# Optimization experiments

Hardware: AMD Instinct MI355X
Metric: run time of the kernel (lower is better)

The kernel has to match this reference:

```python
import jax, jax.numpy as jnp
import numpy as np

DIM, KEY_DIM, HEADS, RATIO, RES = 384, 32, 8, 4, 7
N = RES * RES
D = RATIO * KEY_DIM          # 128 per-head value dim
DH = D * HEADS               # 1024
NHKD = KEY_DIM * HEADS       # 256
SCALE = KEY_DIM ** -0.5


def _make_bias_idxs(res):
    points = [(i, j) for i in range(res) for j in range(res)]
    offsets = {}
    idxs = []
    for p1 in points:
        for p2 in points:
            off = (abs(p1[0] - p2[0]), abs(p1[1] - p2[1]))
            if off not in offsets:
                offsets[off] = len(offsets)
            idxs.append(offsets[off])
    n = len(points)
    return np.asarray(idxs, dtype=np.int32).reshape(n, n), len(offsets)


def setup_inputs() -> dict:
    key = jax.random.key(0)
    ks = jax.random.split(key, 10)
    B = 2048
    idxs_np, n_off = _make_bias_idxs(RES)
    s = 0.02
    return {
        "x": jax.random.normal(ks[0], (B, N, DIM), jnp.float32),
        "q_w": jax.random.normal(ks[1], (NHKD, DIM), jnp.float32) * s,
        "q_b": jnp.zeros((NHKD,), jnp.float32),
        "k_w": jax.random.normal(ks[2], (NHKD, DIM), jnp.float32) * s,
        "k_b": jnp.zeros((NHKD,), jnp.float32),
        "v_w": jax.random.normal(ks[3], (DH, DIM), jnp.float32) * s,
        "v_b": jnp.zeros((DH,), jnp.float32),
        "proj_w": jax.random.normal(ks[4], (DIM, DH), jnp.float32) * s,
        "proj_b": jnp.zeros((DIM,), jnp.float32),
        "attention_biases": jax.random.normal(ks[5], (HEADS, n_off), jnp.float32) * s,
        "bias_idxs": jnp.asarray(idxs_np),  # [N, N] int32
    }


def reference(x, q_w, q_b, k_w, k_b, v_w, v_b, proj_w, proj_b,
              attention_biases, bias_idxs):
    B, n, _ = x.shape
    q = (x @ q_w.T + q_b).reshape(B, n, HEADS, KEY_DIM)
    k = (x @ k_w.T + k_b).reshape(B, n, HEADS, KEY_DIM)
    v = (x @ v_w.T + v_b).reshape(B, n, HEADS, D)
    # learned relative-position bias gathered per (query, key) pair: [H, N, N]
    ab = attention_biases[:, bias_idxs]
    attn = jnp.einsum("bnhd,bmhd->bhnm", q, k) * SCALE + ab
    attn = jax.nn.softmax(attn, axis=-1)
    out = jnp.einsum("bhnm,bmhd->bnhd", attn, v).reshape(B, n, DH)
    return out @ proj_w.T + proj_b
```

## Files before the change

kernel.cpp:

```cpp
#include <hip/hip_runtime.h>
#include <hip/hip_bf16.h>

#define NTOK   49
#define DIM    384
#define KEY_DIM 32
#define HEADS  8
#define D_HEAD 128
#define SCALE  0.17677669529663687f

typedef short short8 __attribute__((ext_vector_type(8)));
typedef short short4_t __attribute__((ext_vector_type(4)));
typedef float f32x4 __attribute__((ext_vector_type(4)));

__device__ __forceinline__ unsigned short f2bf(float x) {
    union { __hip_bfloat16 b; unsigned short u; } v;
    v.b = __float2bfloat16(x);
    return v.u;
}

__device__ __forceinline__ f32x4 MFMA(short8 a, short8 b, f32x4 c) {
    return __builtin_amdgcn_mfma_f32_16x16x32_bf16(a, b, c, 0, 0, 0);
}

__device__ __forceinline__ void bar_lgkm() {
    asm volatile("s_waitcnt lgkmcnt(0)" ::: "memory");
    __builtin_amdgcn_sched_barrier(0);
    __builtin_amdgcn_s_barrier();
    __builtin_amdgcn_sched_barrier(0);
}

__global__ void prologue(const float* __restrict__ qw, const float* __restrict__ qb,
                         const float* __restrict__ kw,
                         const float* __restrict__ vw, const float* __restrict__ pw,
                         const float* __restrict__ biases, const int* __restrict__ idxs,
                         int n_off,
                         unsigned short* __restrict__ qk_p,
                         unsigned short* __restrict__ vw_p,
                         unsigned short* __restrict__ pw_p,
                         float* __restrict__ qb_s,
                         float* __restrict__ ab_t) {
    int t = blockIdx.x * 256 + threadIdx.x;
    if (t < 24576) {
        int lane = t & 63, kt = (t >> 6) % 12, ntile = t / 768;
        int c = ntile * 16 + (lane & 15), kk = kt * 32 + (lane >> 4) * 8;
        const float* src = (c < 256) ? (qw + c * 384 + kk) : (kw + (c - 256) * 384 + kk);
        float sc = (c < 256) ? SCALE : 1.0f;
        short8 o;
#pragma unroll
        for (int j = 0; j < 8; ++j) o[j] = (short)f2bf(src[j] * sc);
        *(short8*)(qk_p + (size_t)t * 8) = o;
    } else if (t < 73728) {
        int u = t - 24576;
        int lane = u & 63, kt = (u >> 6) % 12, ntile = u / 768;
        int c = ntile * 16 + (lane & 15), kk = kt * 32 + (lane >> 4) * 8;
        const float* src = vw + c * 384 + kk;
        short8 o;
#pragma unroll
        for (int j = 0; j < 8; ++j) o[j] = (short)f2bf(src[j]);
        *(short8*)(vw_p + (size_t)u * 8) = o;
    } else if (t < 122880) {
        int u = t - 73728;
        int lane = u & 63, kt = (u >> 6) % 32, ntile = u / 2048;
        int c = ntile * 16 + (lane & 15), kk = kt * 32 + (lane >> 4) * 8;
        const float* src = pw + c * 1024 + kk;
        short8 o;
#pragma unroll
        for (int j = 0; j < 8; ++j) o[j] = (short)f2bf(src[j]);
        *(short8*)(pw_p + (size_t)u * 8) = o;
    } else if (t < 123136) {
        int u = t - 122880;
        qb_s[u] = qb[u] * SCALE;
    } else if (t < 123136 + 32768) {
        int u = t - 123136;
        int h = u >> 12, n = (u >> 6) & 63, m = u & 63;
        float v = 0.f;
        if (m < 49 && n < 49) v = biases[h * n_off + idxs[n * 49 + m]];
        ab_t[u] = v;
    }
}

__global__ __launch_bounds__(512, 4) void attn_qkv(
        const float* __restrict__ x,
        const unsigned short* __restrict__ qkw,
        const unsigned short* __restrict__ vw,
        const float* __restrict__ qb_s, const float* __restrict__ kb,
        const float* __restrict__ vb,
        const float* __restrict__ ab_t,
        unsigned short* __restrict__ O_p) {

    __shared__ __align__(16) unsigned short smem[37072];
    unsigned short* xs  = smem;
    unsigned short* ps  = smem + 19208;
    unsigned short* vsT = smem + 22736;
    unsigned short* qs  = smem + 31952;
    unsigned short* ks2 = smem + 34512;

    const int tid  = threadIdx.x;
    const int lane = tid & 63;
    const int wid  = tid >> 6;
    const int l15  = lane & 15;
    const int lg   = lane >> 4;
    const int b    = blockIdx.x;

    const float* xb = x + (size_t)b * (NTOK * DIM);
#pragma unroll 2
    for (int i = tid; i < 4704; i += 512) {
        f32x4 v = __builtin_nontemporal_load(((const f32x4*)xb) + i);
        int f = i * 4;
        int row = f / DIM;
        int col = f - row * DIM;
        short4_t pk;
        pk[0] = (short)f2bf(v[0]); pk[1] = (short)f2bf(v[1]);
        pk[2] = (short)f2bf(v[2]); pk[3] = (short)f2bf(v[3]);
        *(short4_t*)&xs[row * 392 + col] = pk;
    }
    __syncthreads();

    const f32x4 zf = (f32x4)0.f;

    for (int h = 0; h < HEADS; ++h) {
        {
            const int mh  = wid >> 2;
            const int nt0 = 3 * (wid & 3);
            const int rA0 = min(mh * 32 + l15, 48);
            const int rA1 = min(mh * 32 + 16 + l15, 48);
            f32x4 acc[3][2];
#pragma unroll
            for (int i = 0; i < 3; ++i) { acc[i][0] = zf; acc[i][1] = zf; }

            const short8* bptr[3];
#pragma unroll
            for (int i = 0; i < 3; ++i) {
                int nt = nt0 + i;
                const unsigned short* base; int ntile;
                if (nt < 2)      { base = qkw; ntile = 2 * h + nt; }
                else if (nt < 4) { base = qkw; ntile = 16 + 2 * h + (nt - 2); }
                else             { base = vw;  ntile = 8 * h + (nt - 4); }
                bptr[i] = (const short8*)(base + (size_t)ntile * 12 * 64 * 8);
            }
            __builtin_amdgcn_s_setprio(1);
#pragma unroll
            for (int kt = 0; kt < 12; ++kt) {
                short8 a0 = *(const short8*)&xs[rA0 * 392 + kt * 32 + lg * 8];
                short8 a1 = *(const short8*)&xs[rA1 * 392 + kt * 32 + lg * 8];
#pragma unroll
                for (int i = 0; i < 3; ++i) {
                    short8 bf = bptr[i][kt * 64 + lane];
                    acc[i][0] = MFMA(a0, bf, acc[i][0]);
                    acc[i][1] = MFMA(a1, bf, acc[i][1]);
                }
            }
            __builtin_amdgcn_s_setprio(0);
#pragma unroll
            for (int i = 0; i < 3; ++i) {
                int nt = nt0 + i;
                int c  = nt * 16 + l15;
                if (nt < 4) {
                    int cc = (nt < 2) ? c : c - 32;
                    float bias = (nt < 2) ? qb_s[h * 32 + cc] : kb[h * 32 + cc];
                    unsigned short* dst = (nt < 2) ? qs : ks2;
#pragma unroll
                    for (int j = 0; j < 2; ++j) {
                        int r0 = mh * 32 + j * 16 + lg * 4;
                        f32x4 v = acc[i][j];
#pragma unroll
                        for (int r = 0; r < 4; ++r)
                            dst[(r0 + r) * 40 + cc] = f2bf(v[r] + bias);
                    }
                } else {
                    int d = c - 64;
                    float bias = vb[h * 128 + d];
#pragma unroll
                    for (int j = 0; j < 2; ++j) {
                        int m0 = mh * 32 + j * 16 + lg * 4;
                        f32x4 v = acc[i][j];
                        short4_t pk;
#pragma unroll
                        for (int r = 0; r < 4; ++r) pk[r] = (short)f2bf(v[r] + bias);
                        *(short4_t*)&vsT[d * 72 + m0] = pk;
                    }
                }
            }
        }
        bar_lgkm();

        if (wid < 4) {
            const int I = wid;
            const int rq = min(I * 16 + l15, 48);
            short8 bq = *(const short8*)&qs[rq * 40 + lg * 8];
            f32x4 s[4];
#pragma unroll
            for (int J = 0; J < 4; ++J) {
                short8 ak = *(const short8*)&ks2[(J * 16 + l15) * 40 + lg * 8];
                s[J] = MFMA(ak, bq, zf);
            }
            const f32x4* abn = (const f32x4*)(ab_t + ((h * 64 + I * 16 + l15) * 64));
            float sv[16];
            float mx = -1e30f;
#pragma unroll
            for (int J = 0; J < 4; ++J) {
                f32x4 a4 = abn[J * 4 + lg];
#pragma unroll
                for (int r = 0; r < 4; ++r) {
                    int m = J * 16 + lg * 4 + r;
                    float val = s[J][r] + a4[r];
                    if (m >= 49) val = -1e30f;
                    sv[J * 4 + r] = val;
                    mx = fmaxf(mx, val);
                }
            }
            mx = fmaxf(mx, __shfl_xor(mx, 16));
            mx = fmaxf(mx, __shfl_xor(mx, 32));
            float sum = 0.f;
#pragma unroll
            for (int t = 0; t < 16; ++t) { float e = __expf(sv[t] - mx); sv[t] = e; sum += e; }
            sum += __shfl_xor(sum, 16);
            sum += __shfl_xor(sum, 32);
            float inv = 1.0f / sum;
            int n = I * 16 + l15;
            if (n < 49) {
#pragma unroll
                for (int J = 0; J < 4; ++J)
#pragma unroll
                    for (int r = 0; r < 4; ++r) {
                        int m = J * 16 + lg * 4 + r;
                        ps[n * 72 + m] = f2bf(sv[J * 4 + r] * inv);
                    }
            }
        }
        bar_lgkm();

        {
            const int np = wid >> 2;
            const int dp = wid & 3;
            const int rp0 = min(np * 32 + l15, 48);
            const int rp1 = min(np * 32 + 16 + l15, 48);
            f32x4 a00 = zf, a01 = zf, a10 = zf, a11 = zf;
            __builtin_amdgcn_s_setprio(1);
#pragma unroll
            for (int kk = 0; kk < 2; ++kk) {
                short8 a0 = *(const short8*)&ps[rp0 * 72 + kk * 32 + lg * 8];
                short8 a1 = *(const short8*)&ps[rp1 * 72 + kk * 32 + lg * 8];
                short8 b0 = *(const short8*)&vsT[(dp * 32 + l15) * 72 + kk * 32 + lg * 8];
                short8 b1 = *(const short8*)&vsT[(dp * 32 + 16 + l15) * 72 + kk * 32 + lg * 8];
                a00 = MFMA(a0, b0, a00); a01 = MFMA(a0, b1, a01);
                a10 = MFMA(a1, b0, a10); a11 = MFMA(a1, b1, a11);
            }
            __builtin_amdgcn_s_setprio(0);
            f32x4 accs[2][2] = {{a00, a01}, {a10, a11}};
            unsigned short* ob = O_p + (((size_t)b * 8 + h) * 32) * 256;
#pragma unroll
            for (int jn = 0; jn < 2; ++jn)
#pragma unroll
                for (int jd = 0; jd < 2; ++jd) {
                    int frag = (np * 2 + jn) * 8 + (dp * 2 + jd);
                    f32x4 v = accs[jn][jd];
                    short4_t pk;
#pragma unroll
                    for (int r = 0; r < 4; ++r) pk[r] = (short)f2bf(v[r]);
                    __builtin_nontemporal_store(pk, (short4_t*)(ob + frag * 256 + lane * 4));
                }
        }
        bar_lgkm();
    }
}

#define OPJ_STRIDE 520
__global__ __launch_bounds__(512, 4) void out_proj(
        const unsigned short* __restrict__ O_p,
        const unsigned short* __restrict__ pw,
        const float* __restrict__ pb,
        float* __restrict__ out) {

    __shared__ unsigned short osB[64 * OPJ_STRIDE];

    const int tid  = threadIdx.x;
    const int lane = tid & 63;
    const int wid  = tid >> 6;
    const int l15  = lane & 15;
    const int lg   = lane >> 4;
    const int b    = blockIdx.x;

    const short8* pwp = (const short8*)pw;
    f32x4 acc[3][4];
#pragma unroll
    for (int i = 0; i < 3; ++i)
#pragma unroll
        for (int I = 0; I < 4; ++I) acc[i][I] = (f32x4)0.f;

#pragma unroll
    for (int p = 0; p < 2; ++p) {
        const short8* obase = (const short8*)(O_p + (size_t)b * 65536 + p * 32768);
        short8 vv[8];
#pragma unroll
        for (int it = 0; it < 8; ++it)
            vv[it] = __builtin_nontemporal_load(obase + tid + it * 512);
        if (p) __syncthreads();
#pragma unroll
        for (int it = 0; it < 8; ++it) {
            int s = tid + it * 512;
            int fl0 = s * 2;
            int hl   = fl0 >> 11;
            int frag = (fl0 >> 6) & 31;
            int ln0  = fl0 & 63;
            int mt = frag >> 3, dt = frag & 7;
            short8 v = vv[it];
#pragma unroll
            for (int q = 0; q < 2; ++q) {
                int ln = ln0 + q;
                int n0 = mt * 16 + ((ln >> 4) << 2);
                int d  = hl * 128 + dt * 16 + (ln & 15);
#pragma unroll
                for (int r = 0; r < 4; ++r)
                    osB[(n0 + r) * OPJ_STRIDE + d] = (unsigned short)v[q * 4 + r];
            }
        }
        __syncthreads();

        for (int ktl = 0; ktl < 16; ++ktl) {
            short8 bfr[4];
#pragma unroll
            for (int I = 0; I < 4; ++I)
                bfr[I] = *(const short8*)&osB[(I * 16 + l15) * OPJ_STRIDE + ktl * 32 + lg * 8];
#pragma unroll
            for (int i = 0; i < 3; ++i) {
                short8 a = pwp[((size_t)(wid * 3 + i) * 32 + p * 16 + ktl) * 64 + lane];
#pragma unroll
                for (int I = 0; I < 4; ++I) acc[i][I] = MFMA(a, bfr[I], acc[i][I]);
            }
        }
    }

    float* obaseo = out + (size_t)b * (NTOK * 384);
#pragma unroll
    for (int i = 0; i < 3; ++i) {
        int c0 = (wid * 3 + i) * 16 + lg * 4;
        f32x4 bias4 = *(const f32x4*)&pb[c0];
#pragma unroll
        for (int I = 0; I < 4; ++I) {
            int n = I * 16 + l15;
            if (n < 49) {
                f32x4 v = acc[i][I] + bias4;
                __builtin_nontemporal_store(v, (f32x4*)&obaseo[n * 384 + c0]);
            }
        }
    }
}

__global__ __launch_bounds__(512) void fused_attn(
        const float* __restrict__ x,
        const unsigned short* __restrict__ qkw,
        const unsigned short* __restrict__ vw,
        const unsigned short* __restrict__ pw,
        const float* __restrict__ qb_s, const float* __restrict__ kb,
        const float* __restrict__ vb, const float* __restrict__ pb,
        const float* __restrict__ ab_t,
        float* __restrict__ out) {

    __shared__ __align__(16) unsigned short smem[40656];
    unsigned short* xs  = smem;
    unsigned short* ps  = smem + 19208;
    unsigned short* vsT = smem + 22736;
    unsigned short* qs  = smem + 31952;
    unsigned short* ks2 = smem + 31952 + 2560;
    unsigned short* osA = smem + 31952;

    const int tid  = threadIdx.x;
    const int lane = tid & 63;
    const int wid  = tid >> 6;
    const int l15  = lane & 15;
    const int lg   = lane >> 4;
    const int b    = blockIdx.x;

    const float* xb = x + (size_t)b * (NTOK * DIM);
#pragma unroll 2
    for (int i = tid; i < 4704; i += 512) {
        f32x4 v = __builtin_nontemporal_load(((const f32x4*)xb) + i);
        int f = i * 4;
        int row = f / DIM;
        int col = f - row * DIM;
        short4_t pk;
        pk[0] = (short)f2bf(v[0]); pk[1] = (short)f2bf(v[1]);
        pk[2] = (short)f2bf(v[2]); pk[3] = (short)f2bf(v[3]);
        *(short4_t*)&xs[row * 392 + col] = pk;
    }
    __syncthreads();

    f32x4 pacc[3][4];
#pragma unroll
    for (int i = 0; i < 3; ++i)
#pragma unroll
        for (int j = 0; j < 4; ++j) pacc[i][j] = (f32x4)0.f;

    const f32x4 zf = (f32x4)0.f;

    for (int h = 0; h < HEADS; ++h) {
        {
            const int mh  = wid >> 2;
            const int nt0 = 3 * (wid & 3);
            const int rA0 = min(mh * 32 + l15, 48);
            const int rA1 = min(mh * 32 + 16 + l15, 48);
            f32x4 acc[3][2];
#pragma unroll
            for (int i = 0; i < 3; ++i) { acc[i][0] = zf; acc[i][1] = zf; }

            const short8* bptr[3];
#pragma unroll
            for (int i = 0; i < 3; ++i) {
                int nt = nt0 + i;
                const unsigned short* base; int ntile;
                if (nt < 2)      { base = qkw; ntile = 2 * h + nt; }
                else if (nt < 4) { base = qkw; ntile = 16 + 2 * h + (nt - 2); }
                else             { base = vw;  ntile = 8 * h + (nt - 4); }
                bptr[i] = (const short8*)(base + (size_t)ntile * 12 * 64 * 8);
            }
#pragma unroll
            for (int kt = 0; kt < 12; ++kt) {
                short8 a0 = *(const short8*)&xs[rA0 * 392 + kt * 32 + lg * 8];
                short8 a1 = *(const short8*)&xs[rA1 * 392 + kt * 32 + lg * 8];
#pragma unroll
                for (int i = 0; i < 3; ++i) {
                    short8 bf = bptr[i][kt * 64 + lane];
                    acc[i][0] = MFMA(a0, bf, acc[i][0]);
                    acc[i][1] = MFMA(a1, bf, acc[i][1]);
                }
            }
#pragma unroll
            for (int i = 0; i < 3; ++i) {
                int nt = nt0 + i;
                int c  = nt * 16 + l15;
                if (nt < 4) {
                    int cc = (nt < 2) ? c : c - 32;
                    float bias = (nt < 2) ? qb_s[h * 32 + cc] : kb[h * 32 + cc];
                    unsigned short* dst = (nt < 2) ? qs : ks2;
#pragma unroll
                    for (int j = 0; j < 2; ++j) {
                        int r0 = mh * 32 + j * 16 + lg * 4;
                        f32x4 v = acc[i][j];
#pragma unroll
                        for (int r = 0; r < 4; ++r)
                            dst[(r0 + r) * 40 + cc] = f2bf(v[r] + bias);
                    }
                } else {
                    int d = c - 64;
                    float bias = vb[h * 128 + d];
#pragma unroll
                    for (int j = 0; j < 2; ++j) {
                        int m0 = mh * 32 + j * 16 + lg * 4;
                        f32x4 v = acc[i][j];
                        short4_t pk;
#pragma unroll
                        for (int r = 0; r < 4; ++r) pk[r] = (short)f2bf(v[r] + bias);
                        *(short4_t*)&vsT[d * 72 + m0] = pk;
                    }
                }
            }
        }
        __syncthreads();

        if (wid < 4) {
            const int I = wid;
            const int rq = min(I * 16 + l15, 48);
            short8 bq = *(const short8*)&qs[rq * 40 + lg * 8];
            f32x4 s[4];
#pragma unroll
            for (int J = 0; J < 4; ++J) {
                short8 ak = *(const short8*)&ks2[(J * 16 + l15) * 40 + lg * 8];
                s[J] = MFMA(ak, bq, zf);
            }
            const f32x4* abn = (const f32x4*)(ab_t + ((h * 64 + I * 16 + l15) * 64));
            float sv[16];
            float mx = -1e30f;
#pragma unroll
            for (int J = 0; J < 4; ++J) {
                f32x4 a4 = abn[J * 4 + lg];
#pragma unroll
                for (int r = 0; r < 4; ++r) {
                    int m = J * 16 + lg * 4 + r;
                    float val = s[J][r] + a4[r];
                    if (m >= 49) val = -1e30f;
                    sv[J * 4 + r] = val;
                    mx = fmaxf(mx, val);
                }
            }
            mx = fmaxf(mx, __shfl_xor(mx, 16));
            mx = fmaxf(mx, __shfl_xor(mx, 32));
            float sum = 0.f;
#pragma unroll
            for (int t = 0; t < 16; ++t) { float e = __expf(sv[t] - mx); sv[t] = e; sum += e; }
            sum += __shfl_xor(sum, 16);
            sum += __shfl_xor(sum, 32);
            float inv = 1.0f / sum;
            int n = I * 16 + l15;
            if (n < 49) {
#pragma unroll
                for (int J = 0; J < 4; ++J)
#pragma unroll
                    for (int r = 0; r < 4; ++r) {
                        int m = J * 16 + lg * 4 + r;
                        ps[n * 72 + m] = f2bf(sv[J * 4 + r] * inv);
                    }
            }
        }
        __syncthreads();

        {
            const int np = wid >> 2;
            const int dp = wid & 3;
            const int rp0 = min(np * 32 + l15, 48);
            const int rp1 = min(np * 32 + 16 + l15, 48);
            f32x4 a00 = zf, a01 = zf, a10 = zf, a11 = zf;
#pragma unroll
            for (int kk = 0; kk < 2; ++kk) {
                short8 a0 = *(const short8*)&ps[rp0 * 72 + kk * 32 + lg * 8];
                short8 a1 = *(const short8*)&ps[rp1 * 72 + kk * 32 + lg * 8];
                short8 b0 = *(const short8*)&vsT[(dp * 32 + l15) * 72 + kk * 32 + lg * 8];
                short8 b1 = *(const short8*)&vsT[(dp * 32 + 16 + l15) * 72 + kk * 32 + lg * 8];
                a00 = MFMA(a0, b0, a00); a01 = MFMA(a0, b1, a01);
                a10 = MFMA(a1, b0, a10); a11 = MFMA(a1, b1, a11);
            }
            f32x4 accs[2][2] = {{a00, a01}, {a10, a11}};
#pragma unroll
            for (int jn = 0; jn < 2; ++jn)
#pragma unroll
                for (int jd = 0; jd < 2; ++jd) {
                    int r0 = np * 32 + jn * 16 + lg * 4;
                    int d0 = dp * 32 + jd * 16 + l15;
                    f32x4 v = accs[jn][jd];
#pragma unroll
                    for (int r = 0; r < 4; ++r) osA[(r0 + r) * 136 + d0] = f2bf(v[r]);
                }
        }
        __syncthreads();

        {
            const int nt0 = 3 * wid;
#pragma unroll
            for (int kt = 0; kt < 4; ++kt) {
                short8 a[4];
#pragma unroll
                for (int mi = 0; mi < 4; ++mi)
                    a[mi] = *(const short8*)&osA[(mi * 16 + l15) * 136 + kt * 32 + lg * 8];
#pragma unroll
                for (int i = 0; i < 3; ++i) {
                    short8 bf = ((const short8*)pw)[((size_t)(nt0 + i) * 32 + (h * 4 + kt)) * 64 + lane];
#pragma unroll
                    for (int mi = 0; mi < 4; ++mi)
                        pacc[i][mi] = MFMA(a[mi], bf, pacc[i][mi]);
                }
            }
        }
        __syncthreads();
    }

    float* ob = out + (size_t)b * (NTOK * 384);
#pragma unroll
    for (int i = 0; i < 3; ++i) {
        int c = (3 * wid + i) * 16 + l15;
        float bias = pb[c];
#pragma unroll
        for (int mi = 0; mi < 4; ++mi) {
            f32x4 v = pacc[i][mi];
#pragma unroll
            for (int r = 0; r < 4; ++r) {
                int n = mi * 16 + lg * 4 + r;
                if (n < 49) __builtin_nontemporal_store(v[r] + bias, &ob[n * 384 + c]);
            }
        }
    }
}

extern "C" void kernel_launch(void* const* d_in, const int* in_sizes, int n_in,
                              void* d_out, int out_size, void* d_ws, size_t ws_size,
                              hipStream_t stream) {
    const float* x      = (const float*)d_in[0];
    const float* qw     = (const float*)d_in[1];
    const float* qb     = (const float*)d_in[2];
    const float* kw     = (const float*)d_in[3];
    const float* kb     = (const float*)d_in[4];
    const float* vw     = (const float*)d_in[5];
    const float* vb     = (const float*)d_in[6];
    const float* pw     = (const float*)d_in[7];
    const float* pb     = (const float*)d_in[8];
    const float* biases = (const float*)d_in[9];
    const int*   idxs   = (const int*)d_in[10];
    int n_off = in_sizes[9] / HEADS;

    char* ws = (char*)d_ws;
    unsigned short* qk_p = (unsigned short*)ws;
    unsigned short* vw_p = (unsigned short*)(ws + 393216);
    unsigned short* pw_p = (unsigned short*)(ws + 1179648);
    float*          qb_s = (float*)(ws + 1966080);
    float*          ab_t = (float*)(ws + 1967104);
    unsigned short* O_p  = (unsigned short*)(ws + 2098176);

    const size_t need = 2098176ull + (size_t)2048 * 8 * 32 * 256 * 2;

    prologue<<<609, 256, 0, stream>>>(qw, qb, kw, vw, pw, biases, idxs, n_off,
                                      qk_p, vw_p, pw_p, qb_s, ab_t);
    if (ws_size >= need) {
        attn_qkv<<<2048, 512, 0, stream>>>(x, qk_p, vw_p, qb_s, kb, vb, ab_t, O_p);
        out_proj<<<2048, 512, 0, stream>>>(O_p, pw_p, pb, (float*)d_out);
    } else {
        fused_attn<<<2048, 512, 0, stream>>>(x, qk_p, vw_p, pw_p, qb_s, kb, vb, pb,
                                             ab_t, (float*)d_out);
    }
}
```

Before: 414.8 us.

## Warp-specialize attention heads to overlap projections with softmax and PV

Splits the eight waves into two roles per head. Waves 0-3 run softmax and then the P·V product. Meanwhile waves 4-7 compute the V projection for the current head, and then the Q/K projections for the next head. The Q/K projection for head 0 is hoisted before the loop. This removes one block barrier per head and hides the projection MFMAs behind the softmax and PV phases. The cost is uneven per-wave work and more accumulator registers per wave.

Measured after the change: 435.3 us. 5.0% more time.

```diff
diff --git a/kernel.cpp b/kernel.cpp
--- a/kernel.cpp
+++ b/kernel.cpp
@@ -118,70 +118,36 @@
 
     const f32x4 zf = (f32x4)0.f;
 
+    {
+        const int nt  = wid >> 1;
+        const int mtb = (wid & 1) * 2;
+        const int ntile = (nt < 2) ? nt : (16 + (nt - 2));
+        const short8* bptr = (const short8*)(qkw + (size_t)ntile * 12 * 64 * 8);
+        const int rA0 = min(mtb * 16 + l15, 48);
+        const int rA1 = min(mtb * 16 + 16 + l15, 48);
+        f32x4 a0c = zf, a1c = zf;
+#pragma unroll
+        for (int kt = 0; kt < 12; ++kt) {
+            short8 a0 = *(const short8*)&xs[rA0 * 392 + kt * 32 + lg * 8];
+            short8 a1 = *(const short8*)&xs[rA1 * 392 + kt * 32 + lg * 8];
+            short8 bf = bptr[kt * 64 + lane];
+            a0c = MFMA(a0, bf, a0c);
+            a1c = MFMA(a1, bf, a1c);
+        }
+        const int cc = (nt & 1) * 16 + l15;
+        float bias = (nt < 2) ? qb_s[cc] : kb[cc];
+        unsigned short* dst = (nt < 2) ? qs : ks2;
+        f32x4 accs[2] = {a0c, a1c};
+#pragma unroll
+        for (int j = 0; j < 2; ++j) {
+            int r0 = (mtb + j) * 16 + lg * 4;
+#pragma unroll
+            for (int r = 0; r < 4; ++r)
+                dst[(r0 + r) * 40 + cc] = f2bf(accs[j][r] + bias);
+        }
+    }
+
     for (int h = 0; h < HEADS; ++h) {
-        {
-            const int mh  = wid >> 2;
-            const int nt0 = 3 * (wid & 3);
-            const int rA0 = min(mh * 32 + l15, 48);
-            const int rA1 = min(mh * 32 + 16 + l15, 48);
-            f32x4 acc[3][2];
-#pragma unroll
-            for (int i = 0; i < 3; ++i) { acc[i][0] = zf; acc[i][1] = zf; }
-
-            const short8* bptr[3];
-#pragma unroll
-            for (int i = 0; i < 3; ++i) {
-                int nt = nt0 + i;
-                const unsigned short* base; int ntile;
-                if (nt < 2)      { base = qkw; ntile = 2 * h + nt; }
-                else if (nt < 4) { base = qkw; ntile = 16 + 2 * h + (nt - 2); }
-                else             { base = vw;  ntile = 8 * h + (nt - 4); }
-                bptr[i] = (const short8*)(base + (size_t)ntile * 12 * 64 * 8);
-            }
-            __builtin_amdgcn_s_setprio(1);
-#pragma unroll
-            for (int kt = 0; kt < 12; ++kt) {
-                short8 a0 = *(const short8*)&xs[rA0 * 392 + kt * 32 + lg * 8];
-                short8 a1 = *(const short8*)&xs[rA1 * 392 + kt * 32 + lg * 8];
-#pragma unroll
-                for (int i = 0; i < 3; ++i) {
-                    short8 bf = bptr[i][kt * 64 + lane];
-                    acc[i][0] = MFMA(a0, bf, acc[i][0]);
-                    acc[i][1] = MFMA(a1, bf, acc[i][1]);
-                }
-            }
-            __builtin_amdgcn_s_setprio(0);
-#pragma unroll
-            for (int i = 0; i < 3; ++i) {
-                int nt = nt0 + i;
-                int c  = nt * 16 + l15;
-                if (nt < 4) {
-                    int cc = (nt < 2) ? c : c - 32;
-                    float bias = (nt < 2) ? qb_s[h * 32 + cc] : kb[h * 32 + cc];
-                    unsigned short* dst = (nt < 2) ? qs : ks2;
-#pragma unroll
-                    for (int j = 0; j < 2; ++j) {
-                        int r0 = mh * 32 + j * 16 + lg * 4;
-                        f32x4 v = acc[i][j];
-#pragma unroll
-                        for (int r = 0; r < 4; ++r)
-                            dst[(r0 + r) * 40 + cc] = f2bf(v[r] + bias);
-                    }
-                } else {
-                    int d = c - 64;
-                    float bias = vb[h * 128 + d];
-#pragma unroll
-                    for (int j = 0; j < 2; ++j) {
-                        int m0 = mh * 32 + j * 16 + lg * 4;
-                        f32x4 v = acc[i][j];
-                        short4_t pk;
-#pragma unroll
-                        for (int r = 0; r < 4; ++r) pk[r] = (short)f2bf(v[r] + bias);
-                        *(short4_t*)&vsT[d * 72 + m0] = pk;
-                    }
-                }
-            }
-        }
         bar_lgkm();
 
         if (wid < 4) {
@@ -227,41 +193,120 @@
                         ps[n * 72 + m] = f2bf(sv[J * 4 + r] * inv);
                     }
             }
+        } else {
+            const int w = wid - 4;
+            const short8* bp0 = (const short8*)(vw + (size_t)(8 * h + 2 * w) * 12 * 64 * 8);
+            const short8* bp1 = (const short8*)(vw + (size_t)(8 * h + 2 * w + 1) * 12 * 64 * 8);
+            f32x4 acc[2][4];
+#pragma unroll
+            for (int i = 0; i < 2; ++i)
+#pragma unroll
+                for (int m = 0; m < 4; ++m) acc[i][m] = zf;
+            const int r0 = l15, r1 = 16 + l15, r2 = 32 + l15, r3 = 48;
+            __builtin_amdgcn_s_setprio(1);
+#pragma unroll
+            for (int kt = 0; kt < 12; ++kt) {
+                short8 a0 = *(const short8*)&xs[r0 * 392 + kt * 32 + lg * 8];
+                short8 a1 = *(const short8*)&xs[r1 * 392 + kt * 32 + lg * 8];
+                short8 a2 = *(const short8*)&xs[r2 * 392 + kt * 32 + lg * 8];
+                short8 a3 = *(const short8*)&xs[r3 * 392 + kt * 32 + lg * 8];
+                short8 b0 = bp0[kt * 64 + lane];
+                short8 b1 = bp1[kt * 64 + lane];
+                acc[0][0] = MFMA(a0, b0, acc[0][0]); acc[0][1] = MFMA(a1, b0, acc[0][1]);
+                acc[0][2] = MFMA(a2, b0, acc[0][2]); acc[0][3] = MFMA(a3, b0, acc[0][3]);
+                acc[1][0] = MFMA(a0, b1, acc[1][0]); acc[1][1] = MFMA(a1, b1, acc[1][1]);
+                acc[1][2] = MFMA(a2, b1, acc[1][2]); acc[1][3] = MFMA(a3, b1, acc[1][3]);
+            }
+            __builtin_amdgcn_s_setprio(0);
+#pragma unroll
+            for (int i = 0; i < 2; ++i) {
+                int d = (2 * w + i) * 16 + l15;
+                float bias = vb[h * 128 + d];
+#pragma unroll
+                for (int mt = 0; mt < 4; ++mt) {
+                    int m0 = mt * 16 + lg * 4;
+                    short4_t pk;
+#pragma unroll
+                    for (int r = 0; r < 4; ++r) pk[r] = (short)f2bf(acc[i][mt][r] + bias);
+                    *(short4_t*)&vsT[d * 72 + m0] = pk;
+                }
+            }
         }
         bar_lgkm();
 
-        {
-            const int np = wid >> 2;
-            const int dp = wid & 3;
+        if (wid < 4) {
+            const int np  = wid >> 1;
+            const int dpb = (wid & 1) * 2;
             const int rp0 = min(np * 32 + l15, 48);
             const int rp1 = min(np * 32 + 16 + l15, 48);
-            f32x4 a00 = zf, a01 = zf, a10 = zf, a11 = zf;
+            f32x4 acc[2][2][2];
+#pragma unroll
+            for (int i = 0; i < 2; ++i)
+#pragma unroll
+                for (int jn = 0; jn < 2; ++jn)
+#pragma unroll
+                    for (int jd = 0; jd < 2; ++jd) acc[i][jn][jd] = zf;
             __builtin_amdgcn_s_setprio(1);
 #pragma unroll
             for (int kk = 0; kk < 2; ++kk) {
                 short8 a0 = *(const short8*)&ps[rp0 * 72 + kk * 32 + lg * 8];
                 short8 a1 = *(const short8*)&ps[rp1 * 72 + kk * 32 + lg * 8];
-                short8 b0 = *(const short8*)&vsT[(dp * 32 + l15) * 72 + kk * 32 + lg * 8];
-                short8 b1 = *(const short8*)&vsT[(dp * 32 + 16 + l15) * 72 + kk * 32 + lg * 8];
-                a00 = MFMA(a0, b0, a00); a01 = MFMA(a0, b1, a01);
-                a10 = MFMA(a1, b0, a10); a11 = MFMA(a1, b1, a11);
+#pragma unroll
+                for (int i = 0; i < 2; ++i) {
+                    int dp = dpb + i;
+                    short8 b0 = *(const short8*)&vsT[(dp * 32 + l15) * 72 + kk * 32 + lg * 8];
+                    short8 b1 = *(const short8*)&vsT[(dp * 32 + 16 + l15) * 72 + kk * 32 + lg * 8];
+                    acc[i][0][0] = MFMA(a0, b0, acc[i][0][0]);
+                    acc[i][0][1] = MFMA(a0, b1, acc[i][0][1]);
+                    acc[i][1][0] = MFMA(a1, b0, acc[i][1][0]);
+                    acc[i][1][1] = MFMA(a1, b1, acc[i][1][1]);
+                }
             }
             __builtin_amdgcn_s_setprio(0);
-            f32x4 accs[2][2] = {{a00, a01}, {a10, a11}};
             unsigned short* ob = O_p + (((size_t)b * 8 + h) * 32) * 256;
 #pragma unroll
-            for (int jn = 0; jn < 2; ++jn)
-#pragma unroll
-                for (int jd = 0; jd < 2; ++jd) {
-                    int frag = (np * 2 + jn) * 8 + (dp * 2 + jd);
-                    f32x4 v = accs[jn][jd];
-                    short4_t pk;
-#pragma unroll
-                    for (int r = 0; r < 4; ++r) pk[r] = (short)f2bf(v[r]);
-                    __builtin_nontemporal_store(pk, (short4_t*)(ob + frag * 256 + lane * 4));
-                }
-        }
-        bar_lgkm();
+            for (int i = 0; i < 2; ++i)
+#pragma unroll
+                for (int jn = 0; jn < 2; ++jn)
+#pragma unroll
+                    for (int jd = 0; jd < 2; ++jd) {
+                        int frag = (np * 2 + jn) * 8 + ((dpb + i) * 2 + jd);
+                        f32x4 v = acc[i][jn][jd];
+                        short4_t pk;
+#pragma unroll
+                        for (int r = 0; r < 4; ++r) pk[r] = (short)f2bf(v[r]);
+                        __builtin_nontemporal_store(pk, (short4_t*)(ob + frag * 256 + lane * 4));
+                    }
+        } else if (h < HEADS - 1) {
+            const int hn = h + 1;
+            const int nt = wid - 4;
+            const int ntile = (nt < 2) ? (2 * hn + nt) : (16 + 2 * hn + (nt - 2));
+            const short8* bptr = (const short8*)(qkw + (size_t)ntile * 12 * 64 * 8);
+            f32x4 acc[4];
+#pragma unroll
+            for (int m = 0; m < 4; ++m) acc[m] = zf;
+            const int r0 = l15, r1 = 16 + l15, r2 = 32 + l15, r3 = 48;
+#pragma unroll
+            for (int kt = 0; kt < 12; ++kt) {
+                short8 a0 = *(const short8*)&xs[r0 * 392 + kt * 32 + lg * 8];
+                short8 a1 = *(const short8*)&xs[r1 * 392 + kt * 32 + lg * 8];
+                short8 a2 = *(const short8*)&xs[r2 * 392 + kt * 32 + lg * 8];
+                short8 a3 = *(const short8*)&xs[r3 * 392 + kt * 32 + lg * 8];
+                short8 bf = bptr[kt * 64 + lane];
+                acc[0] = MFMA(a0, bf, acc[0]); acc[1] = MFMA(a1, bf, acc[1]);
+                acc[2] = MFMA(a2, bf, acc[2]); acc[3] = MFMA(a3, bf, acc[3]);
+            }
+            const int cc = (nt & 1) * 16 + l15;
+            float bias = (nt < 2) ? qb_s[hn * 32 + cc] : kb[hn * 32 + cc];
+            unsigned short* dst = (nt < 2) ? qs : ks2;
+#pragma unroll
+            for (int mt = 0; mt < 4; ++mt) {
+                int rr0 = mt * 16 + lg * 4;
+#pragma unroll
+                for (int r = 0; r < 4; ++r)
+                    dst[(rr0 + r) * 40 + cc] = f2bf(acc[mt][r] + bias);
+            }
+        }
     }
 }
 
```

## Process two batch items per attn_qkv block to reuse weight fragments

Applied to the files above, without the earlier changes.

Each attn_qkv block now handles two batch elements: both x tiles are staged in doubled shared memory, and every weight fragment loaded from global memory feeds MFMAs for both items. Softmax now uses all 8 waves (4 per item) instead of leaving half idle, and the PV stage loops over both items. The aim is to halve global weight traffic per item and improve wave utilisation. In exchange the grid is halved, shared memory per block doubles (~148KB), launch bounds drop to 2, and accumulator register pressure doubles, which lowers occupancy.

Result: no change. 420.2 us (+1.3%).

```diff
diff --git a/kernel.cpp b/kernel.cpp
--- a/kernel.cpp
+++ b/kernel.cpp
@@ -79,7 +79,7 @@
     }
 }
 
-__global__ __launch_bounds__(512, 4) void attn_qkv(
+__global__ __launch_bounds__(512, 2) void attn_qkv(
         const float* __restrict__ x,
         const unsigned short* __restrict__ qkw,
         const unsigned short* __restrict__ vw,
@@ -88,31 +88,27 @@
         const float* __restrict__ ab_t,
         unsigned short* __restrict__ O_p) {
 
-    __shared__ __align__(16) unsigned short smem[37072];
-    unsigned short* xs  = smem;
-    unsigned short* ps  = smem + 19208;
-    unsigned short* vsT = smem + 22736;
-    unsigned short* qs  = smem + 31952;
-    unsigned short* ks2 = smem + 34512;
+    __shared__ __align__(16) unsigned short smem[74144];
 
     const int tid  = threadIdx.x;
     const int lane = tid & 63;
     const int wid  = tid >> 6;
     const int l15  = lane & 15;
     const int lg   = lane >> 4;
-    const int b    = blockIdx.x;
-
-    const float* xb = x + (size_t)b * (NTOK * DIM);
-#pragma unroll 2
-    for (int i = tid; i < 4704; i += 512) {
-        f32x4 v = __builtin_nontemporal_load(((const f32x4*)xb) + i);
-        int f = i * 4;
+    const int b0   = blockIdx.x * 2;
+
+    for (int i = tid; i < 9408; i += 512) {
+        int q = (i >= 4704) ? 1 : 0;
+        int j = i - q * 4704;
+        f32x4 v = __builtin_nontemporal_load(
+            ((const f32x4*)(x + (size_t)(b0 + q) * (NTOK * DIM))) + j);
+        int f = j * 4;
         int row = f / DIM;
         int col = f - row * DIM;
         short4_t pk;
         pk[0] = (short)f2bf(v[0]); pk[1] = (short)f2bf(v[1]);
         pk[2] = (short)f2bf(v[2]); pk[3] = (short)f2bf(v[3]);
-        *(short4_t*)&xs[row * 392 + col] = pk;
+        *(short4_t*)&smem[q * 37072 + row * 392 + col] = pk;
     }
     __syncthreads();
 
@@ -124,9 +120,12 @@
             const int nt0 = 3 * (wid & 3);
             const int rA0 = min(mh * 32 + l15, 48);
             const int rA1 = min(mh * 32 + 16 + l15, 48);
-            f32x4 acc[3][2];
-#pragma unroll
-            for (int i = 0; i < 3; ++i) { acc[i][0] = zf; acc[i][1] = zf; }
+            f32x4 accA[3][2], accB[3][2];
+#pragma unroll
+            for (int i = 0; i < 3; ++i) {
+                accA[i][0] = zf; accA[i][1] = zf;
+                accB[i][0] = zf; accB[i][1] = zf;
+            }
 
             const short8* bptr[3];
 #pragma unroll
@@ -141,57 +140,73 @@
             __builtin_amdgcn_s_setprio(1);
 #pragma unroll
             for (int kt = 0; kt < 12; ++kt) {
-                short8 a0 = *(const short8*)&xs[rA0 * 392 + kt * 32 + lg * 8];
-                short8 a1 = *(const short8*)&xs[rA1 * 392 + kt * 32 + lg * 8];
+                short8 bf0 = bptr[0][kt * 64 + lane];
+                short8 bf1 = bptr[1][kt * 64 + lane];
+                short8 bf2 = bptr[2][kt * 64 + lane];
+                short8 a0A = *(const short8*)&smem[rA0 * 392 + kt * 32 + lg * 8];
+                short8 a1A = *(const short8*)&smem[rA1 * 392 + kt * 32 + lg * 8];
+                short8 a0B = *(const short8*)&smem[37072 + rA0 * 392 + kt * 32 + lg * 8];
+                short8 a1B = *(const short8*)&smem[37072 + rA1 * 392 + kt * 32 + lg * 8];
+                accA[0][0] = MFMA(a0A, bf0, accA[0][0]); accA[0][1] = MFMA(a1A, bf0, accA[0][1]);
+                accA[1][0] = MFMA(a0A, bf1, accA[1][0]); accA[1][1] = MFMA(a1A, bf1, accA[1][1]);
+                accA[2][0] = MFMA(a0A, bf2, accA[2][0]); accA[2][1] = MFMA(a1A, bf2, accA[2][1]);
+                accB[0][0] = MFMA(a0B, bf0, accB[0][0]); accB[0][1] = MFMA(a1B, bf0, accB[0][1]);
+                accB[1][0] = MFMA(a0B, bf1, accB[1][0]); accB[1][1] = MFMA(a1B, bf1, accB[1][1]);
+                accB[2][0] = MFMA(a0B, bf2, accB[2][0]); accB[2][1] = MFMA(a1B, bf2, accB[2][1]);
+            }
+            __builtin_amdgcn_s_setprio(0);
+#pragma unroll
+            for (int qq = 0; qq < 2; ++qq) {
+                unsigned short* qsq  = smem + qq * 37072 + 31952;
+                unsigned short* ksq  = smem + qq * 37072 + 34512;
+                unsigned short* vsTq = smem + qq * 37072 + 22736;
 #pragma unroll
                 for (int i = 0; i < 3; ++i) {
-                    short8 bf = bptr[i][kt * 64 + lane];
-                    acc[i][0] = MFMA(a0, bf, acc[i][0]);
-                    acc[i][1] = MFMA(a1, bf, acc[i][1]);
-                }
-            }
-            __builtin_amdgcn_s_setprio(0);
-#pragma unroll
-            for (int i = 0; i < 3; ++i) {
-                int nt = nt0 + i;
-                int c  = nt * 16 + l15;
-                if (nt < 4) {
-                    int cc = (nt < 2) ? c : c - 32;
-                    float bias = (nt < 2) ? qb_s[h * 32 + cc] : kb[h * 32 + cc];
-                    unsigned short* dst = (nt < 2) ? qs : ks2;
-#pragma unroll
-                    for (int j = 0; j < 2; ++j) {
-                        int r0 = mh * 32 + j * 16 + lg * 4;
-                        f32x4 v = acc[i][j];
-#pragma unroll
-                        for (int r = 0; r < 4; ++r)
-                            dst[(r0 + r) * 40 + cc] = f2bf(v[r] + bias);
+                    int nt = nt0 + i;
+                    int c  = nt * 16 + l15;
+                    f32x4* acc = qq ? accB[i] : accA[i];
+                    if (nt < 4) {
+                        int cc = (nt < 2) ? c : c - 32;
+                        float bias = (nt < 2) ? qb_s[h * 32 + cc] : kb[h * 32 + cc];
+                        unsigned short* dst = (nt < 2) ? qsq : ksq;
+#pragma unroll
+                        for (int j = 0; j < 2; ++j) {
+                            int r0 = mh * 32 + j * 16 + lg * 4;
+                            f32x4 v = acc[j];
+#pragma unroll
+                            for (int r = 0; r < 4; ++r)
+                                dst[(r0 + r) * 40 + cc] = f2bf(v[r] + bias);
+                        }
+                    } else {
+                        int d = c - 64;
+                        float bias = vb[h * 128 + d];
+#pragma unroll
+                        for (int j = 0; j < 2; ++j) {
+                            int m0 = mh * 32 + j * 16 + lg * 4;
+                            f32x4 v = acc[j];
+                            short4_t pk;
+#pragma unroll
+                            for (int r = 0; r < 4; ++r) pk[r] = (short)f2bf(v[r] + bias);
+                            *(short4_t*)&vsTq[d * 72 + m0] = pk;
+                        }
                     }
-                } else {
-                    int d = c - 64;
-                    float bias = vb[h * 128 + d];
-#pragma unroll
-                    for (int j = 0; j < 2; ++j) {
-                        int m0 = mh * 32 + j * 16 + lg * 4;
-                        f32x4 v = acc[i][j];
-                        short4_t pk;
-#pragma unroll
-                        for (int r = 0; r < 4; ++r) pk[r] = (short)f2bf(v[r] + bias);
-                        *(short4_t*)&vsT[d * 72 + m0] = pk;
-                    }
                 }
             }
         }
         bar_lgkm();
 
-        if (wid < 4) {
-            const int I = wid;
+        {
+            const int q = wid >> 2;
+            const int I = wid & 3;
+            const unsigned short* qsq = smem + q * 37072 + 31952;
+            const unsigned short* ksq = smem + q * 37072 + 34512;
+            unsigned short* psq = smem + q * 37072 + 19208;
             const int rq = min(I * 16 + l15, 48);
-            short8 bq = *(const short8*)&qs[rq * 40 + lg * 8];
+            short8 bq = *(const short8*)&qsq[rq * 40 + lg * 8];
             f32x4 s[4];
 #pragma unroll
             for (int J = 0; J < 4; ++J) {
-                short8 ak = *(const short8*)&ks2[(J * 16 + l15) * 40 + lg * 8];
+                short8 ak = *(const short8*)&ksq[(J * 16 + l15) * 40 + lg * 8];
                 s[J] = MFMA(ak, bq, zf);
             }
             const f32x4* abn = (const f32x4*)(ab_t + ((h * 64 + I * 16 + l15) * 64));
@@ -224,7 +239,7 @@
 #pragma unroll
                     for (int r = 0; r < 4; ++r) {
                         int m = J * 16 + lg * 4 + r;
-                        ps[n * 72 + m] = f2bf(sv[J * 4 + r] * inv);
+                        psq[n * 72 + m] = f2bf(sv[J * 4 + r] * inv);
                     }
             }
         }
@@ -235,31 +250,36 @@
             const int dp = wid & 3;
             const int rp0 = min(np * 32 + l15, 48);
             const int rp1 = min(np * 32 + 16 + l15, 48);
-            f32x4 a00 = zf, a01 = zf, a10 = zf, a11 = zf;
-            __builtin_amdgcn_s_setprio(1);
-#pragma unroll
-            for (int kk = 0; kk < 2; ++kk) {
-                short8 a0 = *(const short8*)&ps[rp0 * 72 + kk * 32 + lg * 8];
-                short8 a1 = *(const short8*)&ps[rp1 * 72 + kk * 32 + lg * 8];
-                short8 b0 = *(const short8*)&vsT[(dp * 32 + l15) * 72 + kk * 32 + lg * 8];
-                short8 b1 = *(const short8*)&vsT[(dp * 32 + 16 + l15) * 72 + kk * 32 + lg * 8];
-                a00 = MFMA(a0, b0, a00); a01 = MFMA(a0, b1, a01);
-                a10 = MFMA(a1, b0, a10); a11 = MFMA(a1, b1, a11);
-            }
-            __builtin_amdgcn_s_setprio(0);
-            f32x4 accs[2][2] = {{a00, a01}, {a10, a11}};
-            unsigned short* ob = O_p + (((size_t)b * 8 + h) * 32) * 256;
-#pragma unroll
-            for (int jn = 0; jn < 2; ++jn)
-#pragma unroll
-                for (int jd = 0; jd < 2; ++jd) {
-                    int frag = (np * 2 + jn) * 8 + (dp * 2 + jd);
-                    f32x4 v = accs[jn][jd];
-                    short4_t pk;
-#pragma unroll
-                    for (int r = 0; r < 4; ++r) pk[r] = (short)f2bf(v[r]);
-                    __builtin_nontemporal_store(pk, (short4_t*)(ob + frag * 256 + lane * 4));
-                }
+#pragma unroll
+            for (int qq = 0; qq < 2; ++qq) {
+                const unsigned short* psq  = smem + qq * 37072 + 19208;
+                const unsigned short* vsTq = smem + qq * 37072 + 22736;
+                f32x4 a00 = zf, a01 = zf, a10 = zf, a11 = zf;
+                __builtin_amdgcn_s_setprio(1);
+#pragma unroll
+                for (int kk = 0; kk < 2; ++kk) {
+                    short8 a0 = *(const short8*)&psq[rp0 * 72 + kk * 32 + lg * 8];
+                    short8 a1 = *(const short8*)&psq[rp1 * 72 + kk * 32 + lg * 8];
+                    short8 b0 = *(const short8*)&vsTq[(dp * 32 + l15) * 72 + kk * 32 + lg * 8];
+                    short8 b1 = *(const short8*)&vsTq[(dp * 32 + 16 + l15) * 72 + kk * 32 + lg * 8];
+                    a00 = MFMA(a0, b0, a00); a01 = MFMA(a0, b1, a01);
+                    a10 = MFMA(a1, b0, a10); a11 = MFMA(a1, b1, a11);
+                }
+                __builtin_amdgcn_s_setprio(0);
+                f32x4 accs[2][2] = {{a00, a01}, {a10, a11}};
+                unsigned short* ob = O_p + (((size_t)(b0 + qq) * 8 + h) * 32) * 256;
+#pragma unroll
+                for (int jn = 0; jn < 2; ++jn)
+#pragma unroll
+                    for (int jd = 0; jd < 2; ++jd) {
+                        int frag = (np * 2 + jn) * 8 + (dp * 2 + jd);
+                        f32x4 v = accs[jn][jd];
+                        short4_t pk;
+#pragma unroll
+                        for (int r = 0; r < 4; ++r) pk[r] = (short)f2bf(v[r]);
+                        __builtin_nontemporal_store(pk, (short4_t*)(ob + frag * 256 + lane * 4));
+                    }
+            }
         }
         bar_lgkm();
     }
@@ -599,7 +619,7 @@
     prologue<<<609, 256, 0, stream>>>(qw, qb, kw, vw, pw, biases, idxs, n_off,
                                       qk_p, vw_p, pw_p, qb_s, ab_t);
     if (ws_size >= need) {
-        attn_qkv<<<2048, 512, 0, stream>>>(x, qk_p, vw_p, qb_s, kb, vb, ab_t, O_p);
+        attn_qkv<<<1024, 512, 0, stream>>>(x, qk_p, vw_p, qb_s, kb, vb, ab_t, O_p);
         out_proj<<<2048, 512, 0, stream>>>(O_p, pw_p, pb, (float*)d_out);
     } else {
         fused_attn<<<2048, 512, 0, stream>>>(x, qk_p, vw_p, pw_p, qb_s, kb, vb, pb,
```
